# Kernel tuning notes

Hardware: AMD Instinct MI355X
Metric: run time of the kernel (lower is better)

The kernel has to match this reference:

```python
import jax, jax.numpy as jnp
import numpy as np

# SpargeAttn / spas_sage2_attn_meansim block sizes
BLKQ, BLKK = 128, 64
NUM_HEADS = 8
SIMTHRESHD1 = 0.6
CDFTHRESHD = 0.98


def _block_meta(t, blk):
    # t: [B,H,S,D] -> block means [B,H,nb,D] and min-cosine-to-mean per block [B,H,nb]
    B, H, S, D = t.shape
    nb = S // blk
    tb = t.reshape(B, H, nb, blk, D)
    m = tb.mean(axis=3)
    tn = tb / (jnp.linalg.norm(tb, axis=-1, keepdims=True) + 1e-6)
    mn = m / (jnp.linalg.norm(m, axis=-1, keepdims=True) + 1e-6)
    cos = jnp.einsum('bhnkd,bhnd->bhnk', tn, mn)
    return m, cos.min(axis=-1)


def _meansim_sparse_attention(q, k, v, scale):
    # Block-sparse attention with mean-similarity pruning (SpargeAttn meansim).
    qm, qsim = _block_meta(q, BLKQ)          # [B,H,nq,D], [B,H,nq]
    km, ksim = _block_meta(k, BLKK)          # [B,H,nk,D], [B,H,nk]
    q_self = qsim > SIMTHRESHD1              # self-similar Q blocks -> mean is representative
    k_self = ksim > SIMTHRESHD1
    # pooled attention map over block means
    pooled = jax.nn.softmax(jnp.einsum('bhqd,bhkd->bhqk', qm, km) * scale, axis=-1)
    # per Q-block row: keep highest-prob K blocks until cumulative mass >= cdfthreshd
    order = jnp.argsort(-pooled, axis=-1)
    sp = jnp.take_along_axis(pooled, order, axis=-1)
    csum = jnp.cumsum(sp, axis=-1)
    keep_sorted = (csum - sp) < CDFTHRESHD   # always keeps at least the top block
    inv = jnp.argsort(order, axis=-1)
    keep = jnp.take_along_axis(keep_sorted, inv, axis=-1)  # [B,H,nq,nk]
    # conservative fallback: non-self-similar Q/K blocks are never pruned
    block_mask = keep | (~q_self)[..., None] | (~k_self)[:, :, None, :]
    tok_mask = jnp.repeat(jnp.repeat(block_mask, BLKQ, axis=2), BLKK, axis=3)
    s = jnp.einsum('bhqd,bhkd->bhqk', q, k) * scale
    s = jnp.where(tok_mask, s, -jnp.inf)
    p = jax.nn.softmax(s, axis=-1)
    return jnp.einsum('bhqk,bhkd->bhqd', p, v)


def setup_inputs() -> dict:
    key = jax.random.key(0)
    B, L, C = 2, 2048, 512
    ks = jax.random.split(key, 3)
    x = jax.random.normal(ks[0], (B, L, C), jnp.float32)
    Wqkv = jax.random.normal(ks[1], (C, 3 * C), jnp.float32) * (C ** -0.5)
    bqkv = jnp.zeros((3 * C,), jnp.float32)
    Wproj = jax.random.normal(ks[2], (C, C), jnp.float32) * (C ** -0.5)
    bproj = jnp.zeros((C,), jnp.float32)
    return {"x": x, "Wqkv": Wqkv, "bqkv": bqkv, "Wproj": Wproj, "bproj": bproj}


def reference(x, Wqkv, bqkv, Wproj, bproj):
    B, L, C = x.shape
    H = NUM_HEADS
    D = C // H
    scale = D ** -0.5
    qkv = (x @ Wqkv + bqkv).reshape(B, L, 3, H, D)
    qkv = jnp.transpose(qkv, (2, 0, 3, 1, 4))  # [3,B,H,L,D]
    q, k, v = qkv[0], qkv[1], qkv[2]
    o = _meansim_sparse_attention(q, k, v, scale)  # [B,H,L,D]
    o = jnp.transpose(o, (0, 2, 1, 3)).reshape(B, L, C)
    return o @ Wproj + bproj
```

## Files before the change

### kernel.cpp

```cpp
#include <hip/hip_runtime.h>
#include <math.h>

typedef unsigned short ushortT;
typedef unsigned int uintT;
typedef __attribute__((ext_vector_type(8))) short short8;
typedef __attribute__((ext_vector_type(16))) float f32x16;
#define MFMA32(a, b, c) __builtin_amdgcn_mfma_f32_32x32x16_bf16((a), (b), (c), 0, 0, 0)


#define LOG2E 1.4426950408889634f

static __device__ __forceinline__ ushortT f2b(float f) {
    union { float f; uintT u; } v; v.f = f;
    uintT u = v.u;
    u += 0x7fffu + ((u >> 16) & 1u);
    return (ushortT)(u >> 16);
}
static __device__ __forceinline__ uintT pack2(float a, float b) {
    return (uintT)f2b(a) | ((uintT)f2b(b) << 16);
}
static __device__ __forceinline__ uintT pack2t(float a, float b) {
    union { float f; uintT u; } x0, x1; x0.f = a; x1.f = b;
    return __builtin_amdgcn_perm(x1.u, x0.u, 0x07060302u);
}
static __device__ __forceinline__ float blo(uintT u) {
    union { uintT u; float f; } v; v.u = u << 16; return v.f;
}
static __device__ __forceinline__ float bhi(uintT u) {
    union { uintT u; float f; } v; v.u = u & 0xffff0000u; return v.f;
}
static __device__ __forceinline__ f32x16 zero16() {
    f32x16 z;
    #pragma unroll
    for (int i = 0; i < 16; ++i) z[i] = 0.f;
    return z;
}

#define B_N 2
#define H_N 8
#define L_N 2048
#define NQB 16
#define NKB 32

__global__ __launch_bounds__(256) void prep_kernel(
    const float* __restrict__ x, ushortT* __restrict__ xb,
    const float* __restrict__ Wq, ushortT* __restrict__ Wqt,
    const float* __restrict__ Wp, ushortT* __restrict__ Wpt) {
    const int bid = blockIdx.x, t = threadIdx.x;
    __shared__ float tile[32][33];
    if (bid < 2048) {
        int i = (bid * 256 + t) * 4;
        float4 v = *(const float4*)(x + i);
        uint2 o; o.x = pack2(v.x, v.y); o.y = pack2(v.z, v.w);
        *(uint2*)(xb + i) = o;
        return;
    }
    const float* W; ushortT* Wt; int C, c0, r0;
    if (bid < 2816) {
        const int b = bid - 2048;
        W = Wq; Wt = Wqt; C = 1536;
        c0 = (b % 48) * 32; r0 = (b / 48) * 32;
    } else {
        const int b = bid - 2816;
        W = Wp; Wt = Wpt; C = 512;
        c0 = (b & 15) * 32; r0 = (b >> 4) * 32;
    }
    const int tx = t & 31, ty = t >> 5;
    #pragma unroll
    for (int i = 0; i < 4; ++i)
        tile[ty + 8 * i][tx] = W[(size_t)(r0 + ty + 8 * i) * C + c0 + tx];
    __syncthreads();
    #pragma unroll
    for (int i = 0; i < 4; ++i) {
        int rr = ty + 8 * i;
        Wt[(size_t)(c0 + rr) * 512 + r0 + tx] = f2b(tile[tx][rr]);
    }
}

__global__ __launch_bounds__(256) void qkv_gemm_kernel(
    const ushortT* __restrict__ xb, const ushortT* __restrict__ wt,
    const float* __restrict__ bias,
    ushortT* __restrict__ qb, ushortT* __restrict__ kbuf, ushortT* __restrict__ vt,
    float* __restrict__ qm, float* __restrict__ km,
    float* __restrict__ qs, float* __restrict__ ks) {
    __shared__ __align__(16) ushortT As[2][128 * 40];
    __shared__ __align__(16) ushortT Bs[2][64 * 40];
    __shared__ float sumbuf[4][64];
    __shared__ float meanS[2][64];
    __shared__ float wminS[4];
    const int t = threadIdx.x;
    const int l = t & 63, w = t >> 6;
    const int lm = l & 31, lh = l >> 5;
    const int rowbase = blockIdx.y * 128;
    const int colbase = blockIdx.x * 64;

    f32x16 acc[2];
    acc[0] = zero16(); acc[1] = zero16();

    const int r = t >> 1, half = t & 1;
    const ushortT* Ag = xb + (size_t)(rowbase + r) * 512 + half * 16;
    const int soA = r * 40 + half * 16;
    const int rb = t >> 2, q4 = t & 3;
    const ushortT* Bg = wt + (size_t)(colbase + rb) * 512 + q4 * 8;
    const int soB = rb * 40 + q4 * 8;

    uint4 a0, a1, b0;
    a0 = *(const uint4*)(Ag); a1 = *(const uint4*)(Ag + 8);
    b0 = *(const uint4*)(Bg);
    *(uint4*)(&As[0][soA]) = a0; *(uint4*)(&As[0][soA] + 8) = a1;
    *(uint4*)(&Bs[0][soB]) = b0;

    for (int k0 = 0; k0 < 512; k0 += 32) {
        const int cur = (k0 >> 5) & 1;
        __syncthreads();
        if (k0 < 480) {
            a0 = *(const uint4*)(Ag + k0 + 32); a1 = *(const uint4*)(Ag + k0 + 40);
            b0 = *(const uint4*)(Bg + k0 + 32);
        }
        #pragma unroll
        for (int ks2 = 0; ks2 < 2; ++ks2) {
            const int ko = 16 * ks2 + 8 * lh;
            short8 af  = *(const short8*)(&As[cur][(32 * w + lm) * 40 + ko]);
            short8 b_0 = *(const short8*)(&Bs[cur][lm * 40 + ko]);
            short8 b_1 = *(const short8*)(&Bs[cur][(32 + lm) * 40 + ko]);
            acc[0] = MFMA32(af, b_0, acc[0]);
            acc[1] = MFMA32(af, b_1, acc[1]);
        }
        if (k0 < 480) {
            const int nxt = cur ^ 1;
            *(uint4*)(&As[nxt][soA]) = a0; *(uint4*)(&As[nxt][soA] + 8) = a1;
            *(uint4*)(&Bs[nxt][soB]) = b0;
        }
    }

    const int which = blockIdx.x >> 3;
    const int h = blockIdx.x & 7;
    const int by = blockIdx.y;
    const int b = by >> 4;
    const size_t hb = (size_t)(b * 8 + h);
    float bias2[2];
    #pragma unroll
    for (int nt = 0; nt < 2; ++nt) bias2[nt] = bias[colbase + 32 * nt + lm];
    float msum[2] = {0.f, 0.f};
    #pragma unroll
    for (int nt = 0; nt < 2; ++nt) {
        const int dd = 32 * nt + lm;
        #pragma unroll
        for (int rg = 0; rg < 16; ++rg) {
            const int row_local = 32 * w + (rg & 3) + 8 * (rg >> 2) + 4 * lh;
            const int ll = (rowbase + row_local) & 2047;
            float val = acc[nt][rg] + bias2[nt];
            if (which == 0) {
                val *= 0.125f;
                msum[nt] += val;
                qb[(hb * 2048 + ll) * 64 + dd] = f2b(val * LOG2E);
            } else if (which == 1) {
                msum[nt] += val;
                kbuf[(hb * 2048 + ll) * 64 + dd] = f2b(val);
            } else {
                vt[hb * 131072 + (size_t)(ll >> 6) * 4096 + dd * 64 + (ll & 63)] = f2b(val);
            }
            acc[nt][rg] = val;
        }
    }
    if (which == 2) return;
    #pragma unroll
    for (int nt = 0; nt < 2; ++nt) {
        float s = msum[nt] + __shfl_xor(msum[nt], 32);
        if (l < 32) sumbuf[w][32 * nt + lm] = s;
    }
    __syncthreads();
    if (which == 0) {
        if (t < 64) {
            const int qbi = by & 15;
            const float m =
                (sumbuf[0][t] + sumbuf[1][t] + sumbuf[2][t] + sumbuf[3][t]) * (1.0f / 128.0f);
            qm[(hb * 16 + qbi) * 64 + t] = m;
            meanS[0][t] = m;
        }
    } else {
        if (t < 128) {
            const int d = t & 63, pair = t >> 6;
            const int kbi = 2 * (by & 15) + pair;
            const float m =
                (sumbuf[2 * pair][d] + sumbuf[2 * pair + 1][d]) * (1.0f / 64.0f);
            km[(hb * 32 + kbi) * 64 + d] = m;
            meanS[pair][d] = m;
        }
    }
    __syncthreads();
    {
        const int mrow = (which == 0) ? 0 : (w >> 1);
        const float mv0 = meanS[mrow][lm], mv1 = meanS[mrow][32 + lm];
        float mn2 = mv0 * mv0 + mv1 * mv1;
        #pragma unroll
        for (int off = 1; off < 32; off <<= 1) mn2 += __shfl_xor(mn2, off);
        const float mnorm = sqrtf(mn2);
        float cmin = 1e30f;
        #pragma unroll
        for (int rg = 0; rg < 16; ++rg) {
            float dp = acc[0][rg] * mv0 + acc[1][rg] * mv1;
            float nn = acc[0][rg] * acc[0][rg] + acc[1][rg] * acc[1][rg];
            #pragma unroll
            for (int off = 1; off < 32; off <<= 1) {
                dp += __shfl_xor(dp, off);
                nn += __shfl_xor(nn, off);
            }
            const float cosv = dp / ((sqrtf(nn) + 1e-6f) * (mnorm + 1e-6f));
            cmin = fminf(cmin, cosv);
        }
        cmin = fminf(cmin, __shfl_xor(cmin, 32));
        if (l == 0) wminS[w] = cmin;
    }
    __syncthreads();
    if (t == 0) {
        if (which == 0) {
            qs[hb * 16 + (by & 15)] =
                fminf(fminf(wminS[0], wminS[1]), fminf(wminS[2], wminS[3]));
        } else {
            ks[hb * 32 + 2 * (by & 15)]     = fminf(wminS[0], wminS[1]);
            ks[hb * 32 + 2 * (by & 15) + 1] = fminf(wminS[2], wminS[3]);
        }
    }
}

#define KS_SH (128 * 72)
#define VS_SH (64 * 136)
__global__ __launch_bounds__(512, 2) void attn_kernel(
    const ushortT* __restrict__ qb, const ushortT* __restrict__ kbuf,
    const ushortT* __restrict__ vt,
    const float* __restrict__ qm, const float* __restrict__ km,
    const float* __restrict__ qs, const float* __restrict__ ks,
    ushortT* __restrict__ ob) {
    __shared__ __align__(16) ushortT smem[2 * KS_SH + 2 * VS_SH];
    __shared__ int klist[33];
    __shared__ float qmS[64];
    __shared__ float pnS[32];
    ushortT (*Ks)[KS_SH] = (ushortT(*)[KS_SH])smem;
    ushortT (*Vs)[VS_SH] = (ushortT(*)[VS_SH])(smem + 2 * KS_SH);

    const int t = threadIdx.x;
    const int l = t & 63, w = t >> 6;
    const int lm = l & 31, lh = l >> 5;
    const int qc = w >> 2, kq = w & 3;
    const int bh = blockIdx.x, qt = blockIdx.y;

    if (t < 64) qmS[t] = qm[((size_t)bh * 16 + qt) * 64 + t];

    const ushortT* qg = qb + ((size_t)bh * 2048 + qt * 128) * 64;
    short8 qf[4][2];
    #pragma unroll
    for (int qh = 0; qh < 2; ++qh)
        #pragma unroll
        for (int ksd = 0; ksd < 4; ++ksd)
            qf[ksd][qh] = *(const short8*)(qg + (64 * qc + 32 * qh + lm) * 64 + 16 * ksd + 8 * lh);
    __syncthreads();

    if (w == 0 && l < 32) {
        const float* kmr = km + ((size_t)bh * 32 + l) * 64;
        float dot = 0.f;
        #pragma unroll
        for (int d = 0; d < 64; ++d) dot += qmS[d] * kmr[d];
        float mx = dot;
        #pragma unroll
        for (int off = 1; off < 32; off <<= 1) mx = fmaxf(mx, __shfl_xor(mx, off));
        const float e = expf(dot - mx);
        float sum = e;
        #pragma unroll
        for (int off = 1; off < 32; off <<= 1) sum += __shfl_xor(sum, off);
        const float pn = e * (1.0f / sum);
        pnS[l] = pn;
        float before = 0.f;
        #pragma unroll
        for (int j = 0; j < 32; ++j) {
            const float pj = pnS[j];
            if (pj > pn || (pj == pn && j < l)) before += pj;
        }
        const bool qfb = !(qs[bh * 16 + qt] > 0.6f);
        const bool kfb = !(ks[bh * 32 + l] > 0.6f);
        const bool keep = (before < 0.98f) || qfb || kfb;
        unsigned long long bal = __ballot(keep);
        if (keep) {
            const int rank = __popcll(bal & ((1ULL << l) - 1ULL));
            klist[rank] = l;
        }
        if (l == 0) klist[32] = __popcll(bal);
    }
    __syncthreads();

    const int cnt = klist[32];
    const int nIter = (cnt + 1) >> 1;

    const int tile = t >> 7, tt = t & 127;
    const int isV = tile >> 1, skh = tile & 1;
    const int srow = tt >> 1, shalf = (tt & 1) * 32;
    const ushortT* gsrc = (isV ? vt : kbuf) + (size_t)bh * 131072;
    const int goff = srow * 64 + shalf;
    const int soff = isV ? (srow * 136 + skh * 64 + shalf)
                         : ((skh * 64 + srow) * 72 + shalf);
    ushortT* sd0 = (isV ? &Vs[0][soff] : &Ks[0][soff]);
    ushortT* sd1 = (isV ? &Vs[1][soff] : &Ks[1][soff]);

    f32x16 oacc[2][2];
    oacc[0][0] = zero16(); oacc[1][0] = zero16();
    oacc[0][1] = zero16(); oacc[1][1] = zero16();
    float l_i[2] = {0.f, 0.f};

    uint4 st0, st1, st2, st3;
    {
        int kidx = skh; if (kidx >= cnt) kidx = cnt - 1;
        const ushortT* g = gsrc + (size_t)klist[kidx] * 4096 + goff;
        st0 = *(const uint4*)(g);      st1 = *(const uint4*)(g + 8);
        st2 = *(const uint4*)(g + 16); st3 = *(const uint4*)(g + 24);
        *(uint4*)(sd0)      = st0; *(uint4*)(sd0 + 8)  = st1;
        *(uint4*)(sd0 + 16) = st2; *(uint4*)(sd0 + 24) = st3;
    }

    for (int i = 0; i < nIter; ++i) {
        const int cur = i & 1;
        __syncthreads();
        if (i + 1 < nIter) {
            int kidx = 2 * (i + 1) + skh; if (kidx >= cnt) kidx = cnt - 1;
            const ushortT* g = gsrc + (size_t)klist[kidx] * 4096 + goff;
            st0 = *(const uint4*)(g);      st1 = *(const uint4*)(g + 8);
            st2 = *(const uint4*)(g + 16); st3 = *(const uint4*)(g + 24);
        }
        const float mf = (2 * i + (kq >> 1) < cnt) ? 1.f : 0.f;
        f32x16 sacc[2];
        sacc[0] = zero16(); sacc[1] = zero16();
        #pragma unroll
        for (int ksd = 0; ksd < 4; ++ksd) {
            const int ko = 16 * ksd + 8 * lh;
            short8 kf = *(const short8*)(&Ks[cur][(32 * kq + lm) * 72 + ko]);
            sacc[0] = MFMA32(kf, qf[ksd][0], sacc[0]);
            sacc[1] = MFMA32(kf, qf[ksd][1], sacc[1]);
        }
        uintT uu[2][4][2];
        #pragma unroll
        for (int qh = 0; qh < 2; ++qh) {
            float psum0 = 0.f, psum1 = 0.f;
            #pragma unroll
            for (int rp = 0; rp < 8; ++rp) {
                const float e0 = __builtin_amdgcn_exp2f(sacc[qh][2 * rp]) * mf;
                const float e1 = __builtin_amdgcn_exp2f(sacc[qh][2 * rp + 1]) * mf;
                psum0 += e0; psum1 += e1;
                uu[qh][rp >> 1][rp & 1] = pack2t(e0, e1);
            }
            float psum = psum0 + psum1;
            psum += __shfl_xor(psum, 32);
            l_i[qh] += psum;
        }
        #pragma unroll
        for (int ksk = 0; ksk < 2; ++ksk) {
            const int vko = 32 * kq + 16 * ksk + 8 * lh;
            short8 vf0 = *(const short8*)(&Vs[cur][lm * 136 + vko]);
            short8 vf1 = *(const short8*)(&Vs[cur][(32 + lm) * 136 + vko]);
            #pragma unroll
            for (int qh = 0; qh < 2; ++qh) {
                const uintT kA = lh ? uu[qh][2 * ksk + 1][0] : uu[qh][2 * ksk][0];
                const uintT kB = lh ? uu[qh][2 * ksk + 1][1] : uu[qh][2 * ksk][1];
                const uintT sA = lh ? uu[qh][2 * ksk][0] : uu[qh][2 * ksk + 1][0];
                const uintT sB = lh ? uu[qh][2 * ksk][1] : uu[qh][2 * ksk + 1][1];
                const uintT rA = (uintT)__shfl_xor((int)sA, 32);
                const uintT rB = (uintT)__shfl_xor((int)sB, 32);
                union { uintT u[4]; short8 v; } cv;
                if (lh == 0) { cv.u[0] = kA; cv.u[1] = kB; cv.u[2] = rA; cv.u[3] = rB; }
                else         { cv.u[0] = rA; cv.u[1] = rB; cv.u[2] = kA; cv.u[3] = kB; }
                oacc[0][qh] = MFMA32(vf0, cv.v, oacc[0][qh]);
                oacc[1][qh] = MFMA32(vf1, cv.v, oacc[1][qh]);
            }
        }
        if (i + 1 < nIter) {
            ushortT* sd = (cur ^ 1) ? sd1 : sd0;
            *(uint4*)(sd)      = st0; *(uint4*)(sd + 8)  = st1;
            *(uint4*)(sd + 16) = st2; *(uint4*)(sd + 24) = st3;
        }
    }

    uint4* ox = (uint4*)smem;
    float* lx = (float*)((char*)smem + 49152);
    __syncthreads();
    if (kq != 0) {
        const int wslot = qc * 3 + (kq - 1);
        #pragma unroll
        for (int dt = 0; dt < 2; ++dt)
            #pragma unroll
            for (int qh = 0; qh < 2; ++qh)
                #pragma unroll
                for (int g2 = 0; g2 < 2; ++g2) {
                    uint4 u;
                    u.x = pack2(oacc[dt][qh][8 * g2 + 0], oacc[dt][qh][8 * g2 + 1]);
                    u.y = pack2(oacc[dt][qh][8 * g2 + 2], oacc[dt][qh][8 * g2 + 3]);
                    u.z = pack2(oacc[dt][qh][8 * g2 + 4], oacc[dt][qh][8 * g2 + 5]);
                    u.w = pack2(oacc[dt][qh][8 * g2 + 6], oacc[dt][qh][8 * g2 + 7]);
                    ox[(wslot * 8 + (dt * 4 + qh * 2 + g2)) * 64 + l] = u;
                }
        if (lh == 0) {
            lx[(wslot * 2 + 0) * 32 + lm] = l_i[0];
            lx[(wslot * 2 + 1) * 32 + lm] = l_i[1];
        }
    }
    __syncthreads();
    if (kq == 0) {
        float lt[2] = {l_i[0], l_i[1]};
        #pragma unroll
        for (int p = 0; p < 3; ++p) {
            const int ws2 = qc * 3 + p;
            lt[0] += lx[(ws2 * 2 + 0) * 32 + lm];
            lt[1] += lx[(ws2 * 2 + 1) * 32 + lm];
            #pragma unroll
            for (int dt = 0; dt < 2; ++dt)
                #pragma unroll
                for (int qh = 0; qh < 2; ++qh)
                    #pragma unroll
                    for (int g2 = 0; g2 < 2; ++g2) {
                        uint4 u = ox[(ws2 * 8 + (dt * 4 + qh * 2 + g2)) * 64 + l];
                        oacc[dt][qh][8 * g2 + 0] += blo(u.x);
                        oacc[dt][qh][8 * g2 + 1] += bhi(u.x);
                        oacc[dt][qh][8 * g2 + 2] += blo(u.y);
                        oacc[dt][qh][8 * g2 + 3] += bhi(u.y);
                        oacc[dt][qh][8 * g2 + 4] += blo(u.z);
                        oacc[dt][qh][8 * g2 + 5] += bhi(u.z);
                        oacc[dt][qh][8 * g2 + 6] += blo(u.w);
                        oacc[dt][qh][8 * g2 + 7] += bhi(u.w);
                    }
        }
        #pragma unroll
        for (int qh = 0; qh < 2; ++qh) {
            const float inv = 1.0f / lt[qh];
            const int token = qt * 128 + qc * 64 + 32 * qh + lm;
            ushortT* orow = ob + ((size_t)bh * 2048 + token) * 64;
            #pragma unroll
            for (int dt = 0; dt < 2; ++dt)
                #pragma unroll
                for (int rp = 0; rp < 8; ++rp) {
                    const int d0 = 32 * dt + 8 * (rp >> 1) + 4 * lh + 2 * (rp & 1);
                    *(uintT*)(orow + d0) =
                        pack2(oacc[dt][qh][2 * rp] * inv, oacc[dt][qh][2 * rp + 1] * inv);
                }
        }
    }
}

__global__ __launch_bounds__(256) void proj_gemm_kernel(
    const ushortT* __restrict__ ob, const ushortT* __restrict__ wpt,
    const float* __restrict__ bias, float* __restrict__ out) {
    __shared__ __align__(16) ushortT As[2][64 * 40];
    __shared__ __align__(16) ushortT Bs[2][64 * 40];
    const int t = threadIdx.x;
    const int l = t & 63, w = t >> 6;
    const int lm = l & 31, lh = l >> 5;
    const int rh = w & 1, ch = w >> 1;
    const int rowbase = blockIdx.y * 64;
    const int colbase = blockIdx.x * 64;

    f32x16 acc = zero16();

    const int r = t >> 2, q4 = t & 3;
    const int token = rowbase + r;
    const int b2 = token >> 11, lt = token & 2047;
    const int so = r * 40 + q4 * 8;
    const ushortT* obbase = ob + ((size_t)(b2 * 8) * 2048 + lt) * 64 + q4 * 8;
    const ushortT* Bg = wpt + (size_t)(colbase + r) * 512 + q4 * 8;

    uint4 a0, b0;
    a0 = *(const uint4*)(obbase);
    b0 = *(const uint4*)(Bg);
    *(uint4*)(&As[0][so]) = a0;
    *(uint4*)(&Bs[0][so]) = b0;

    for (int k0 = 0; k0 < 512; k0 += 32) {
        const int cur = (k0 >> 5) & 1;
        __syncthreads();
        if (k0 < 480) {
            const int kn = k0 + 32;
            const ushortT* Ag = obbase + (size_t)(kn >> 6) * 131072 + (kn & 63);
            a0 = *(const uint4*)(Ag);
            b0 = *(const uint4*)(Bg + kn);
        }
        #pragma unroll
        for (int ks2 = 0; ks2 < 2; ++ks2) {
            const int ko = 16 * ks2 + 8 * lh;
            short8 af = *(const short8*)(&As[cur][(32 * rh + lm) * 40 + ko]);
            short8 bf = *(const short8*)(&Bs[cur][(32 * ch + lm) * 40 + ko]);
            acc = MFMA32(af, bf, acc);
        }
        if (k0 < 480) {
            const int nxt = cur ^ 1;
            *(uint4*)(&As[nxt][so]) = a0;
            *(uint4*)(&Bs[nxt][so]) = b0;
        }
    }
    const int c = colbase + 32 * ch + lm;
    const float bb = bias[c];
    #pragma unroll
    for (int rg = 0; rg < 16; ++rg) {
        const int row_local = 32 * rh + (rg & 3) + 8 * (rg >> 2) + 4 * lh;
        out[(size_t)(rowbase + row_local) * 512 + c] = acc[rg] + bb;
    }
}

extern "C" void kernel_launch(void* const* d_in, const int* in_sizes, int n_in,
                              void* d_out, int out_size, void* d_ws, size_t ws_size,
                              hipStream_t stream) {
    const float* x     = (const float*)d_in[0];
    const float* Wqkv  = (const float*)d_in[1];
    const float* bqkv  = (const float*)d_in[2];
    const float* Wproj = (const float*)d_in[3];
    const float* bproj = (const float*)d_in[4];
    float* out = (float*)d_out;

    char* w = (char*)d_ws;
    ushortT* xb     = (ushortT*)(w);
    ushortT* wqkvt  = (ushortT*)(w + 4194304);
    ushortT* wprojt = (ushortT*)(w + 5767168);
    ushortT* qb     = (ushortT*)(w + 6291456);
    ushortT* kbuf   = (ushortT*)(w + 10485760);
    ushortT* vt     = (ushortT*)(w + 14680064);
    ushortT* ob     = (ushortT*)(w + 18874368);
    float*   qm     = (float*)(w + 23068672);
    float*   km     = (float*)(w + 23134208);
    float*   qs     = (float*)(w + 36406272);
    float*   ks     = (float*)(w + 36407296);

    prep_kernel<<<3072, 256, 0, stream>>>(x, xb, Wqkv, wqkvt, Wproj, wprojt);
    qkv_gemm_kernel<<<dim3(24, 32), 256, 0, stream>>>(xb, wqkvt, bqkv, qb, kbuf, vt,
                                                      qm, km, qs, ks);
    attn_kernel<<<dim3(16, 16), 512, 0, stream>>>(qb, kbuf, vt, qm, km, qs, ks, ob);
    proj_gemm_kernel<<<dim3(8, 64), 256, 0, stream>>>(ob, wprojt, bproj, out);
}
```

Measured before the change: 135.4 us.

## Fuse x bf16 conversion into QKV GEMM and process four K blocks per attention iteration

The separate conversion of x to bf16 in the prep kernel is removed. The QKV GEMM now loads fp32 x directly and packs it to bf16 while staging it into shared memory, which saves one full read/write pass over x. The attention kernel now stages four selected K/V blocks per pipeline stage instead of two, with each warp handling 64 keys in two sub-chunks. This halves the number of barriers and iterations, but it doubles shared memory per stage and wastes more work when the kept-block count is not a multiple of four.

```diff
diff --git a/kernel.cpp b/kernel.cpp
--- a/kernel.cpp
+++ b/kernel.cpp
@@ -36,32 +36,21 @@
     return z;
 }
 
-#define B_N 2
-#define H_N 8
-#define L_N 2048
 #define NQB 16
 #define NKB 32
 
 __global__ __launch_bounds__(256) void prep_kernel(
-    const float* __restrict__ x, ushortT* __restrict__ xb,
     const float* __restrict__ Wq, ushortT* __restrict__ Wqt,
     const float* __restrict__ Wp, ushortT* __restrict__ Wpt) {
     const int bid = blockIdx.x, t = threadIdx.x;
     __shared__ float tile[32][33];
-    if (bid < 2048) {
-        int i = (bid * 256 + t) * 4;
-        float4 v = *(const float4*)(x + i);
-        uint2 o; o.x = pack2(v.x, v.y); o.y = pack2(v.z, v.w);
-        *(uint2*)(xb + i) = o;
-        return;
-    }
     const float* W; ushortT* Wt; int C, c0, r0;
-    if (bid < 2816) {
-        const int b = bid - 2048;
+    if (bid < 768) {
+        const int b = bid;
         W = Wq; Wt = Wqt; C = 1536;
         c0 = (b % 48) * 32; r0 = (b / 48) * 32;
     } else {
-        const int b = bid - 2816;
+        const int b = bid - 768;
         W = Wp; Wt = Wpt; C = 512;
         c0 = (b & 15) * 32; r0 = (b >> 4) * 32;
     }
@@ -78,7 +67,7 @@
 }
 
 __global__ __launch_bounds__(256) void qkv_gemm_kernel(
-    const ushortT* __restrict__ xb, const ushortT* __restrict__ wt,
+    const float* __restrict__ x, const ushortT* __restrict__ wt,
     const float* __restrict__ bias,
     ushortT* __restrict__ qb, ushortT* __restrict__ kbuf, ushortT* __restrict__ vt,
     float* __restrict__ qm, float* __restrict__ km,
@@ -98,24 +87,30 @@
     acc[0] = zero16(); acc[1] = zero16();
 
     const int r = t >> 1, half = t & 1;
-    const ushortT* Ag = xb + (size_t)(rowbase + r) * 512 + half * 16;
+    const float* Agf = x + (size_t)(rowbase + r) * 512 + half * 16;
     const int soA = r * 40 + half * 16;
     const int rb = t >> 2, q4 = t & 3;
     const ushortT* Bg = wt + (size_t)(colbase + rb) * 512 + q4 * 8;
     const int soB = rb * 40 + q4 * 8;
 
-    uint4 a0, a1, b0;
-    a0 = *(const uint4*)(Ag); a1 = *(const uint4*)(Ag + 8);
+    float4 af0, af1, af2, af3; uint4 b0;
+    af0 = *(const float4*)(Agf);     af1 = *(const float4*)(Agf + 4);
+    af2 = *(const float4*)(Agf + 8); af3 = *(const float4*)(Agf + 12);
     b0 = *(const uint4*)(Bg);
-    *(uint4*)(&As[0][soA]) = a0; *(uint4*)(&As[0][soA] + 8) = a1;
+    *(uint4*)(&As[0][soA]) = make_uint4(pack2(af0.x, af0.y), pack2(af0.z, af0.w),
+                                        pack2(af1.x, af1.y), pack2(af1.z, af1.w));
+    *(uint4*)(&As[0][soA] + 8) = make_uint4(pack2(af2.x, af2.y), pack2(af2.z, af2.w),
+                                            pack2(af3.x, af3.y), pack2(af3.z, af3.w));
     *(uint4*)(&Bs[0][soB]) = b0;
 
     for (int k0 = 0; k0 < 512; k0 += 32) {
         const int cur = (k0 >> 5) & 1;
         __syncthreads();
         if (k0 < 480) {
-            a0 = *(const uint4*)(Ag + k0 + 32); a1 = *(const uint4*)(Ag + k0 + 40);
-            b0 = *(const uint4*)(Bg + k0 + 32);
+            const int kn = k0 + 32;
+            af0 = *(const float4*)(Agf + kn);      af1 = *(const float4*)(Agf + kn + 4);
+            af2 = *(const float4*)(Agf + kn + 8);  af3 = *(const float4*)(Agf + kn + 12);
+            b0 = *(const uint4*)(Bg + kn);
         }
         #pragma unroll
         for (int ks2 = 0; ks2 < 2; ++ks2) {
@@ -128,7 +123,10 @@
         }
         if (k0 < 480) {
             const int nxt = cur ^ 1;
-            *(uint4*)(&As[nxt][soA]) = a0; *(uint4*)(&As[nxt][soA] + 8) = a1;
+            *(uint4*)(&As[nxt][soA]) = make_uint4(pack2(af0.x, af0.y), pack2(af0.z, af0.w),
+                                                  pack2(af1.x, af1.y), pack2(af1.z, af1.w));
+            *(uint4*)(&As[nxt][soA] + 8) = make_uint4(pack2(af2.x, af2.y), pack2(af2.z, af2.w),
+                                                      pack2(af3.x, af3.y), pack2(af3.z, af3.w));
             *(uint4*)(&Bs[nxt][soB]) = b0;
         }
     }
@@ -224,8 +222,8 @@
     }
 }
 
-#define KS_SH (128 * 72)
-#define VS_SH (64 * 136)
+#define KS_SH (256 * 72)
+#define VS_SH (64 * 264)
 __global__ __launch_bounds__(512, 2) void attn_kernel(
     const ushortT* __restrict__ qb, const ushortT* __restrict__ kbuf,
     const ushortT* __restrict__ vt,
@@ -289,91 +287,118 @@
     __syncthreads();
 
     const int cnt = klist[32];
-    const int nIter = (cnt + 1) >> 1;
-
-    const int tile = t >> 7, tt = t & 127;
-    const int isV = tile >> 1, skh = tile & 1;
-    const int srow = tt >> 1, shalf = (tt & 1) * 32;
-    const ushortT* gsrc = (isV ? vt : kbuf) + (size_t)bh * 131072;
-    const int goff = srow * 64 + shalf;
-    const int soff = isV ? (srow * 136 + skh * 64 + shalf)
-                         : ((skh * 64 + srow) * 72 + shalf);
-    ushortT* sd0 = (isV ? &Vs[0][soff] : &Ks[0][soff]);
-    ushortT* sd1 = (isV ? &Vs[1][soff] : &Ks[1][soff]);
+    const int nIter = (cnt + 3) >> 2;
+
+    const ushortT* kgb = kbuf + (size_t)bh * 131072;
+    const ushortT* vgb = vt + (size_t)bh * 131072;
+
+    const int isV = t >> 8, tt = t & 255;
+    int slotA, goffA, soffA, slotB, goffB, soffB;
+    if (!isV) {
+        const int hf = (tt & 1) * 32, rA = tt >> 1, rB = rA + 128;
+        slotA = rA >> 6; goffA = (rA & 63) * 64 + hf; soffA = rA * 72 + hf;
+        slotB = rB >> 6; goffB = (rB & 63) * 64 + hf; soffB = rB * 72 + hf;
+    } else {
+        const int hf = (tt & 1) * 32, qp = tt >> 6, d = (tt & 63) >> 1;
+        slotA = qp; goffA = d * 64 + hf;        soffA = d * 264 + qp * 64 + hf;
+        slotB = qp; goffB = (d + 32) * 64 + hf; soffB = (d + 32) * 264 + qp * 64 + hf;
+    }
+    const ushortT* gsrc = isV ? vgb : kgb;
+    ushortT* sA0 = isV ? &Vs[0][0] : &Ks[0][0];
+    ushortT* sA1 = isV ? &Vs[1][0] : &Ks[1][0];
 
     f32x16 oacc[2][2];
     oacc[0][0] = zero16(); oacc[1][0] = zero16();
     oacc[0][1] = zero16(); oacc[1][1] = zero16();
     float l_i[2] = {0.f, 0.f};
 
-    uint4 st0, st1, st2, st3;
+    uint4 st[8];
     {
-        int kidx = skh; if (kidx >= cnt) kidx = cnt - 1;
-        const ushortT* g = gsrc + (size_t)klist[kidx] * 4096 + goff;
-        st0 = *(const uint4*)(g);      st1 = *(const uint4*)(g + 8);
-        st2 = *(const uint4*)(g + 16); st3 = *(const uint4*)(g + 24);
-        *(uint4*)(sd0)      = st0; *(uint4*)(sd0 + 8)  = st1;
-        *(uint4*)(sd0 + 16) = st2; *(uint4*)(sd0 + 24) = st3;
+        int ka = slotA; if (ka >= cnt) ka = cnt - 1;
+        int kb2 = slotB; if (kb2 >= cnt) kb2 = cnt - 1;
+        const ushortT* gA = gsrc + (size_t)klist[ka] * 4096 + goffA;
+        const ushortT* gB = gsrc + (size_t)klist[kb2] * 4096 + goffB;
+        st[0] = *(const uint4*)(gA);      st[1] = *(const uint4*)(gA + 8);
+        st[2] = *(const uint4*)(gA + 16); st[3] = *(const uint4*)(gA + 24);
+        st[4] = *(const uint4*)(gB);      st[5] = *(const uint4*)(gB + 8);
+        st[6] = *(const uint4*)(gB + 16); st[7] = *(const uint4*)(gB + 24);
+        *(uint4*)(sA0 + soffA)      = st[0]; *(uint4*)(sA0 + soffA + 8)  = st[1];
+        *(uint4*)(sA0 + soffA + 16) = st[2]; *(uint4*)(sA0 + soffA + 24) = st[3];
+        *(uint4*)(sA0 + soffB)      = st[4]; *(uint4*)(sA0 + soffB + 8)  = st[5];
+        *(uint4*)(sA0 + soffB + 16) = st[6]; *(uint4*)(sA0 + soffB + 24) = st[7];
     }
 
     for (int i = 0; i < nIter; ++i) {
         const int cur = i & 1;
         __syncthreads();
         if (i + 1 < nIter) {
-            int kidx = 2 * (i + 1) + skh; if (kidx >= cnt) kidx = cnt - 1;
-            const ushortT* g = gsrc + (size_t)klist[kidx] * 4096 + goff;
-            st0 = *(const uint4*)(g);      st1 = *(const uint4*)(g + 8);
-            st2 = *(const uint4*)(g + 16); st3 = *(const uint4*)(g + 24);
-        }
-        const float mf = (2 * i + (kq >> 1) < cnt) ? 1.f : 0.f;
-        f32x16 sacc[2];
-        sacc[0] = zero16(); sacc[1] = zero16();
-        #pragma unroll
-        for (int ksd = 0; ksd < 4; ++ksd) {
-            const int ko = 16 * ksd + 8 * lh;
-            short8 kf = *(const short8*)(&Ks[cur][(32 * kq + lm) * 72 + ko]);
-            sacc[0] = MFMA32(kf, qf[ksd][0], sacc[0]);
-            sacc[1] = MFMA32(kf, qf[ksd][1], sacc[1]);
-        }
-        uintT uu[2][4][2];
-        #pragma unroll
-        for (int qh = 0; qh < 2; ++qh) {
-            float psum0 = 0.f, psum1 = 0.f;
+            int ka = 4 * (i + 1) + slotA; if (ka >= cnt) ka = cnt - 1;
+            int kb2 = 4 * (i + 1) + slotB; if (kb2 >= cnt) kb2 = cnt - 1;
+            const ushortT* gA = gsrc + (size_t)klist[ka] * 4096 + goffA;
+            const ushortT* gB = gsrc + (size_t)klist[kb2] * 4096 + goffB;
+            st[0] = *(const uint4*)(gA);      st[1] = *(const uint4*)(gA + 8);
+            st[2] = *(const uint4*)(gA + 16); st[3] = *(const uint4*)(gA + 24);
+            st[4] = *(const uint4*)(gB);      st[5] = *(const uint4*)(gB + 8);
+            st[6] = *(const uint4*)(gB + 16); st[7] = *(const uint4*)(gB + 24);
+        }
+        auto process = [&](const float mfv) {
             #pragma unroll
-            for (int rp = 0; rp < 8; ++rp) {
-                const float e0 = __builtin_amdgcn_exp2f(sacc[qh][2 * rp]) * mf;
-                const float e1 = __builtin_amdgcn_exp2f(sacc[qh][2 * rp + 1]) * mf;
-                psum0 += e0; psum1 += e1;
-                uu[qh][rp >> 1][rp & 1] = pack2t(e0, e1);
+            for (int kh = 0; kh < 2; ++kh) {
+                f32x16 sacc[2];
+                sacc[0] = zero16(); sacc[1] = zero16();
+                #pragma unroll
+                for (int ksd = 0; ksd < 4; ++ksd) {
+                    const int ko = 16 * ksd + 8 * lh;
+                    short8 kf = *(const short8*)(&Ks[cur][(64 * kq + 32 * kh + lm) * 72 + ko]);
+                    sacc[0] = MFMA32(kf, qf[ksd][0], sacc[0]);
+                    sacc[1] = MFMA32(kf, qf[ksd][1], sacc[1]);
+                }
+                uintT uu[2][4][2];
+                #pragma unroll
+                for (int qh = 0; qh < 2; ++qh) {
+                    float psum0 = 0.f, psum1 = 0.f;
+                    #pragma unroll
+                    for (int rp = 0; rp < 8; ++rp) {
+                        const float e0 = __builtin_amdgcn_exp2f(sacc[qh][2 * rp]) * mfv;
+                        const float e1 = __builtin_amdgcn_exp2f(sacc[qh][2 * rp + 1]) * mfv;
+                        psum0 += e0; psum1 += e1;
+                        uu[qh][rp >> 1][rp & 1] = pack2t(e0, e1);
+                    }
+                    float psum = psum0 + psum1;
+                    psum += __shfl_xor(psum, 32);
+                    l_i[qh] += psum;
+                }
+                #pragma unroll
+                for (int ksk = 0; ksk < 2; ++ksk) {
+                    const int vko = 64 * kq + 32 * kh + 16 * ksk + 8 * lh;
+                    short8 vf0 = *(const short8*)(&Vs[cur][lm * 264 + vko]);
+                    short8 vf1 = *(const short8*)(&Vs[cur][(32 + lm) * 264 + vko]);
+                    #pragma unroll
+                    for (int qh = 0; qh < 2; ++qh) {
+                        const uintT kA = lh ? uu[qh][2 * ksk + 1][0] : uu[qh][2 * ksk][0];
+                        const uintT kB = lh ? uu[qh][2 * ksk + 1][1] : uu[qh][2 * ksk][1];
+                        const uintT sA = lh ? uu[qh][2 * ksk][0] : uu[qh][2 * ksk + 1][0];
+                        const uintT sB = lh ? uu[qh][2 * ksk][1] : uu[qh][2 * ksk + 1][1];
+                        const uintT rA = (uintT)__shfl_xor((int)sA, 32);
+                        const uintT rB = (uintT)__shfl_xor((int)sB, 32);
+                        union { uintT u[4]; short8 v; } cv;
+                        if (lh == 0) { cv.u[0] = kA; cv.u[1] = kB; cv.u[2] = rA; cv.u[3] = rB; }
+                        else         { cv.u[0] = rA; cv.u[1] = rB; cv.u[2] = kA; cv.u[3] = kB; }
+                        oacc[0][qh] = MFMA32(vf0, cv.v, oacc[0][qh]);
+                        oacc[1][qh] = MFMA32(vf1, cv.v, oacc[1][qh]);
+                    }
+                }
             }
-            float psum = psum0 + psum1;
-            psum += __shfl_xor(psum, 32);
-            l_i[qh] += psum;
-        }
-        #pragma unroll
-        for (int ksk = 0; ksk < 2; ++ksk) {
-            const int vko = 32 * kq + 16 * ksk + 8 * lh;
-            short8 vf0 = *(const short8*)(&Vs[cur][lm * 136 + vko]);
-            short8 vf1 = *(const short8*)(&Vs[cur][(32 + lm) * 136 + vko]);
-            #pragma unroll
-            for (int qh = 0; qh < 2; ++qh) {
-                const uintT kA = lh ? uu[qh][2 * ksk + 1][0] : uu[qh][2 * ksk][0];
-                const uintT kB = lh ? uu[qh][2 * ksk + 1][1] : uu[qh][2 * ksk][1];
-                const uintT sA = lh ? uu[qh][2 * ksk][0] : uu[qh][2 * ksk + 1][0];
-                const uintT sB = lh ? uu[qh][2 * ksk][1] : uu[qh][2 * ksk + 1][1];
-                const uintT rA = (uintT)__shfl_xor((int)sA, 32);
-                const uintT rB = (uintT)__shfl_xor((int)sB, 32);
-                union { uintT u[4]; short8 v; } cv;
-                if (lh == 0) { cv.u[0] = kA; cv.u[1] = kB; cv.u[2] = rA; cv.u[3] = rB; }
-                else         { cv.u[0] = rA; cv.u[1] = rB; cv.u[2] = kA; cv.u[3] = kB; }
-                oacc[0][qh] = MFMA32(vf0, cv.v, oacc[0][qh]);
-                oacc[1][qh] = MFMA32(vf1, cv.v, oacc[1][qh]);
-            }
-        }
+        };
+        if (4 * i + 4 <= cnt) process(1.f);
+        else                  process((4 * i + kq < cnt) ? 1.f : 0.f);
+
         if (i + 1 < nIter) {
-            ushortT* sd = (cur ^ 1) ? sd1 : sd0;
-            *(uint4*)(sd)      = st0; *(uint4*)(sd + 8)  = st1;
-            *(uint4*)(sd + 16) = st2; *(uint4*)(sd + 24) = st3;
+            ushortT* sd = cur ? sA0 : sA1;
+            *(uint4*)(sd + soffA)      = st[0]; *(uint4*)(sd + soffA + 8)  = st[1];
+            *(uint4*)(sd + soffA + 16) = st[2]; *(uint4*)(sd + soffA + 24) = st[3];
+            *(uint4*)(sd + soffB)      = st[4]; *(uint4*)(sd + soffB + 8)  = st[5];
+            *(uint4*)(sd + soffB + 16) = st[6]; *(uint4*)(sd + soffB + 24) = st[7];
         }
     }
 
@@ -511,7 +536,6 @@
     float* out = (float*)d_out;
 
     char* w = (char*)d_ws;
-    ushortT* xb     = (ushortT*)(w);
     ushortT* wqkvt  = (ushortT*)(w + 4194304);
     ushortT* wprojt = (ushortT*)(w + 5767168);
     ushortT* qb     = (ushortT*)(w + 6291456);
@@ -523,8 +547,8 @@
     float*   qs     = (float*)(w + 36406272);
     float*   ks     = (float*)(w + 36407296);
 
-    prep_kernel<<<3072, 256, 0, stream>>>(x, xb, Wqkv, wqkvt, Wproj, wprojt);
-    qkv_gemm_kernel<<<dim3(24, 32), 256, 0, stream>>>(xb, wqkvt, bqkv, qb, kbuf, vt,
+    prep_kernel<<<1024, 256, 0, stream>>>(Wqkv, wqkvt, Wproj, wprojt);
+    qkv_gemm_kernel<<<dim3(24, 32), 256, 0, stream>>>(x, wqkvt, bqkv, qb, kbuf, vt,
                                                       qm, km, qs, ks);
     attn_kernel<<<dim3(16, 16), 512, 0, stream>>>(qb, kbuf, vt, qm, km, qs, ks, ob);
     proj_gemm_kernel<<<dim3(8, 64), 256, 0, stream>>>(ob, wprojt, bproj, out);
```

Measured after the change: 170.0 us. +25.5%, slower.
